# Kernel tuning notes

Hardware: AMD Instinct MI355X
Metric: run time of the kernel (lower is better)

## Reference

```python
import jax, jax.numpy as jnp
import numpy as np

N, E = 50000, 800000
D_IN, D_E = 256, 64
H1, H2 = 128, 128
N_OUT = 64
LEAKY_SLOPE = 0.01  # torch.nn.LeakyReLU default
EPS = 1e-16         # PyG softmax denominator eps


def setup_inputs() -> dict:
    key = jax.random.key(0)
    ks = jax.random.split(key, 32)

    def w(k, shape, s=0.05):
        return jax.random.normal(k, shape, dtype=jnp.float32) * s

    inp = {
        "x_in": jax.random.normal(ks[0], (N, D_IN), dtype=jnp.float32),
        "edge_index": jax.random.randint(ks[1], (2, E), 0, N),
        "edge_atts": jax.random.normal(ks[2], (E, D_E), dtype=jnp.float32),
        # TransformerConv layer 1 (in=D_IN, out=H1, heads=1, beta=True, edge_dim=D_E)
        "Wq1": w(ks[3], (H1, D_IN)), "bq1": jnp.zeros((H1,), jnp.float32),
        "Wk1": w(ks[4], (H1, D_IN)), "bk1": jnp.zeros((H1,), jnp.float32),
        "Wv1": w(ks[5], (H1, D_IN)), "bv1": jnp.zeros((H1,), jnp.float32),
        "We1": w(ks[6], (H1, D_E)),                     # lin_edge (bias=False)
        "Wskip1": w(ks[7], (H1, D_IN)), "bskip1": jnp.zeros((H1,), jnp.float32),
        "Wbeta1": w(ks[8], (1, 3 * H1)),                # lin_beta (bias=False)
        # TransformerConv layer 2 (in=H1, out=H2)
        "Wq2": w(ks[9], (H2, H1)), "bq2": jnp.zeros((H2,), jnp.float32),
        "Wk2": w(ks[10], (H2, H1)), "bk2": jnp.zeros((H2,), jnp.float32),
        "Wv2": w(ks[11], (H2, H1)), "bv2": jnp.zeros((H2,), jnp.float32),
        "We2": w(ks[12], (H2, D_E)),
        "Wskip2": w(ks[13], (H2, H1)), "bskip2": jnp.zeros((H2,), jnp.float32),
        "Wbeta2": w(ks[14], (1, 3 * H2)),
        # output MLP: Linear(H1 + H2 -> N_OUT)
        "Wm": w(ks[15], (N_OUT, H1 + H2)), "bm": jnp.zeros((N_OUT,), jnp.float32),
    }
    return inp


def _transformer_conv(x, src, dst, edge_attr,
                      Wq, bq, Wk, bk, Wv, bv, We, Wskip, bskip, Wbeta, n_nodes):
    """PyG TransformerConv: heads=1, concat=True, beta=True, root_weight=True,
    dropout inactive (eval mode)."""
    d = Wq.shape[0]
    q = x @ Wq.T + bq                      # [N, d]
    k = x @ Wk.T + bk                      # [N, d]
    v = x @ Wv.T + bv                      # [N, d]
    e = edge_attr @ We.T                   # [E, d]
    k_e = k[src] + e                       # gather source keys + edge embedding
    v_e = v[src] + e                       # gather source values + edge embedding
    # attention score per edge
    score = jnp.einsum('ed,ed->e', q[dst], k_e) / jnp.sqrt(jnp.asarray(d, jnp.float32))
    # segment softmax over incoming edges of each destination node
    m = jax.ops.segment_max(score, dst, num_segments=n_nodes)
    m = jnp.where(jnp.isfinite(m), m, 0.0)
    ex = jnp.exp(score - m[dst])
    denom = jax.ops.segment_sum(ex, dst, num_segments=n_nodes) + EPS
    alpha = ex / denom[dst]                # [E]
    # scatter-add weighted messages
    out = jax.ops.segment_sum(alpha[:, None] * v_e, dst, num_segments=n_nodes)  # [N, d]
    # beta-gated skip connection
    x_r = x @ Wskip.T + bskip
    beta = jax.nn.sigmoid(jnp.concatenate([out, x_r, out - x_r], axis=1) @ Wbeta.T)  # [N, 1]
    return beta * x_r + (1.0 - beta) * out


def _leaky_relu(x):
    return jnp.where(x >= 0, x, LEAKY_SLOPE * x)


def reference(x_in, edge_index, edge_atts,
              Wq1, bq1, Wk1, bk1, Wv1, bv1, We1, Wskip1, bskip1, Wbeta1,
              Wq2, bq2, Wk2, bk2, Wv2, bv2, We2, Wskip2, bskip2, Wbeta2,
              Wm, bm):
    src, dst = edge_index[0], edge_index[1]
    n = x_in.shape[0]
    x1 = _leaky_relu(_transformer_conv(x_in, src, dst, edge_atts,
                                       Wq1, bq1, Wk1, bk1, Wv1, bv1, We1,
                                       Wskip1, bskip1, Wbeta1, n))
    x2 = _leaky_relu(_transformer_conv(x1, src, dst, edge_atts,
                                       Wq2, bq2, Wk2, bk2, Wv2, bv2, We2,
                                       Wskip2, bskip2, Wbeta2, n))
    out = jnp.concatenate([x1, x2], axis=1) @ Wm.T + bm   # [N, N_OUT]
    return out
```

## Files before the change

kernel.cpp:

```cpp
#include <hip/hip_runtime.h>
#include <hip/hip_bf16.h>
#include <math.h>

typedef unsigned short u16;
typedef unsigned int u32;
typedef __attribute__((ext_vector_type(8))) short bf16x8;
typedef __attribute__((ext_vector_type(4))) float f32x4;

__device__ inline u16 f2bf(float x) {
    unsigned u = __float_as_uint(x);
    unsigned r = u + 0x7fff + ((u >> 16) & 1);
    return (u16)(r >> 16);
}
__device__ inline float bf2f(u16 h) { return __uint_as_float(((unsigned)h) << 16); }
__device__ inline void bsplit(float x, u16& h, u16& l) {
    h = f2bf(x);
    float r = x - bf2f(h);
    l = f2bf(r);
}

__global__ void count_deg(const int* __restrict__ dst, int* __restrict__ cnt, int E) {
    int e = blockIdx.x * blockDim.x + threadIdx.x;
    if (e < E) atomicAdd(&cnt[dst[e]], 1);
}

__global__ __launch_bounds__(1024) void scan_a(const int* __restrict__ cnt,
                                               int* __restrict__ out,
                                               int* __restrict__ partials, int N) {
    __shared__ int sh[1024];
    int tid = threadIdx.x;
    int gid = blockIdx.x * 1024 + tid;
    int v = (gid < N) ? cnt[gid] : 0;
    sh[tid] = v;
    for (int off = 1; off < 1024; off <<= 1) {
        __syncthreads();
        int add = (tid >= off) ? sh[tid - off] : 0;
        __syncthreads();
        sh[tid] += add;
    }
    __syncthreads();
    if (gid <= N) out[gid] = sh[tid] - v;
    if (tid == 1023) partials[blockIdx.x] = sh[1023];
}

__global__ void scan_b(int* __restrict__ partials, int nb) {
    if (threadIdx.x == 0 && blockIdx.x == 0) {
        int run = 0;
        for (int i = 0; i < nb; ++i) { int t = partials[i]; partials[i] = run; run += t; }
    }
}

__global__ __launch_bounds__(1024) void scan_c(int* __restrict__ out,
                                               const int* __restrict__ partials,
                                               int* __restrict__ fillb, int N) {
    int gid = blockIdx.x * 1024 + threadIdx.x;
    if (gid <= N) {
        int v = out[gid] + partials[blockIdx.x];
        out[gid] = v;
        fillb[gid] = v;
    }
}

__global__ void fill_edges(const int* __restrict__ src, const int* __restrict__ dst,
                           int* __restrict__ fillb, int2* __restrict__ esi, int E) {
    int e = blockIdx.x * blockDim.x + threadIdx.x;
    if (e < E) {
        int d = dst[e];
        int slot = atomicAdd(&fillb[d], 1);
        esi[slot] = make_int2(src[e], e);
    }
}

__global__ __launch_bounds__(256) void prep_weights(
    const float* __restrict__ Wq1, const float* __restrict__ Wk1,
    const float* __restrict__ Wv1, const float* __restrict__ Ws1,
    const float* __restrict__ We1,
    const float* __restrict__ bq1, const float* __restrict__ bk1,
    const float* __restrict__ bv1, const float* __restrict__ bs1,
    const float* __restrict__ Wq2, const float* __restrict__ Wk2,
    const float* __restrict__ Wv2, const float* __restrict__ Ws2,
    const float* __restrict__ We2,
    const float* __restrict__ bq2, const float* __restrict__ bk2,
    const float* __restrict__ bv2, const float* __restrict__ bs2,
    const float* __restrict__ Wm,
    u16* __restrict__ Wc1H, u16* __restrict__ Wc1L,
    u16* __restrict__ Wc2H, u16* __restrict__ Wc2L,
    float* __restrict__ bcat1, float* __restrict__ bcat2,
    float* __restrict__ WeT1, float* __restrict__ WeT2,
    u16* __restrict__ WmH, u16* __restrict__ WmL) {
    int b = blockIdx.x;
    int t = threadIdx.x;
    if (b < 1152) {
        int L = b / 576;
        int r = b - L * 576;
        int K = L ? 128 : 256;
        const float* Wq = L ? Wq2 : Wq1;
        const float* We = L ? We2 : We1;
        u16* WH = L ? Wc2H : Wc1H;
        u16* WL = L ? Wc2L : Wc1L;
        float* bcat = L ? bcat2 : bcat1;
        float val = 0.f;
        bool have = t < K;
        if (r < 512) {
            int sub = r >> 7, rr = r & 127;
            const float* Wsrc = L ? (sub == 0 ? Wq2 : sub == 1 ? Wk2 : sub == 2 ? Wv2 : Ws2)
                                  : (sub == 0 ? Wq1 : sub == 1 ? Wk1 : sub == 2 ? Wv1 : Ws1);
            if (have) val = Wsrc[(size_t)rr * K + t];
            if (t == 0) {
                const float* bsrc = L ? (sub == 0 ? bq2 : sub == 1 ? bk2 : sub == 2 ? bv2 : bs2)
                                      : (sub == 0 ? bq1 : sub == 1 ? bk1 : sub == 2 ? bv1 : bs1);
                bcat[r] = bsrc[rr];
            }
        } else {
            int o = r - 512;
            if (have) {
                float s = 0.f;
                for (int h = 0; h < 128; ++h)
                    s = fmaf(We[h * 64 + o], Wq[(size_t)h * K + t], s);
                val = s;
            }
            if (t == 0) {
                const float* bq = L ? bq2 : bq1;
                float sb = 0.f;
                for (int h = 0; h < 128; ++h) sb = fmaf(We[h * 64 + o], bq[h], sb);
                bcat[r] = sb;
            }
        }
        if (have) {
            u16 h, l;
            bsplit(val, h, l);
            WH[(size_t)r * K + t] = h;
            WL[(size_t)r * K + t] = l;
        }
    } else if (b == 1152 || b == 1153) {
        const float* We = (b == 1152) ? We1 : We2;
        float* WeT = (b == 1152) ? WeT1 : WeT2;
        for (int i = t; i < 128 * 64; i += 256)
            WeT[(i & 63) * 128 + (i >> 6)] = We[i];
    } else {
        for (int i = t; i < 64 * 256; i += 256) {
            u16 h, l;
            bsplit(Wm[i], h, l);
            WmH[i] = h;
            WmL[i] = l;
        }
    }
}

__global__ void split_planes(const float* __restrict__ src, u16* __restrict__ hi,
                             u16* __restrict__ lo, int n4) {
    int i = (blockIdx.x * blockDim.x + threadIdx.x) * 4;
    if (i < n4) {
        float4 v = *reinterpret_cast<const float4*>(&src[i]);
        u16 h0, h1, h2, h3, l0, l1, l2, l3;
        bsplit(v.x, h0, l0); bsplit(v.y, h1, l1);
        bsplit(v.z, h2, l2); bsplit(v.w, h3, l3);
        *reinterpret_cast<ushort4*>(&hi[i]) = make_ushort4(h0, h1, h2, h3);
        *reinterpret_cast<ushort4*>(&lo[i]) = make_ushort4(l0, l1, l2, l3);
    }
}

#define BM 128
#define BO 64
#define BKX 64
#define LSTR 72
__global__ __launch_bounds__(256) void gemm_mfma(
    const u16* __restrict__ XH, const u16* __restrict__ XL, int ldx,
    const u16* __restrict__ WH, const u16* __restrict__ WL,
    const float* __restrict__ bias, float* __restrict__ Out, int ldo,
    int Nrows, int K) {
    __shared__ __align__(16) u16 XsH[BM * LSTR];
    __shared__ __align__(16) u16 XsL[BM * LSTR];
    __shared__ __align__(16) u16 WsH[BO * LSTR];
    __shared__ __align__(16) u16 WsL[BO * LSTR];
    int n0 = blockIdx.x * BM, o0 = blockIdx.y * BO;
    int t = threadIdx.x, wid = t >> 6, lane = t & 63;
    int xr = t >> 1, xk = (t & 1) * 32;
    int wr = t >> 2, wk = (t & 3) * 16;
    bool xok = (n0 + xr) < Nrows;
    const u16* xh = XH + (size_t)(n0 + xr) * ldx + xk;
    const u16* xl = XL + (size_t)(n0 + xr) * ldx + xk;
    const u16* wh = WH + (size_t)(o0 + wr) * K + wk;
    const u16* wl = WL + (size_t)(o0 + wr) * K + wk;
    f32x4 acc[2][4] = {};
    for (int k0 = 0; k0 < K; k0 += BKX) {
#pragma unroll
        for (int j = 0; j < 4; ++j) {
            bf16x8 vh = {0, 0, 0, 0, 0, 0, 0, 0};
            bf16x8 vl = {0, 0, 0, 0, 0, 0, 0, 0};
            if (xok) {
                vh = *reinterpret_cast<const bf16x8*>(xh + k0 + 8 * j);
                vl = *reinterpret_cast<const bf16x8*>(xl + k0 + 8 * j);
            }
            *reinterpret_cast<bf16x8*>(&XsH[xr * LSTR + xk + 8 * j]) = vh;
            *reinterpret_cast<bf16x8*>(&XsL[xr * LSTR + xk + 8 * j]) = vl;
        }
#pragma unroll
        for (int j = 0; j < 2; ++j) {
            *reinterpret_cast<bf16x8*>(&WsH[wr * LSTR + wk + 8 * j]) =
                *reinterpret_cast<const bf16x8*>(wh + k0 + 8 * j);
            *reinterpret_cast<bf16x8*>(&WsL[wr * LSTR + wk + 8 * j]) =
                *reinterpret_cast<const bf16x8*>(wl + k0 + 8 * j);
        }
        __syncthreads();
#pragma unroll
        for (int kc = 0; kc < 2; ++kc) {
            int kf = kc * 32 + (lane >> 4) * 8;
            int ar = wid * 32 + (lane & 15);
            bf16x8 aH0 = *reinterpret_cast<const bf16x8*>(&XsH[ar * LSTR + kf]);
            bf16x8 aH1 = *reinterpret_cast<const bf16x8*>(&XsH[(ar + 16) * LSTR + kf]);
            bf16x8 aL0 = *reinterpret_cast<const bf16x8*>(&XsL[ar * LSTR + kf]);
            bf16x8 aL1 = *reinterpret_cast<const bf16x8*>(&XsL[(ar + 16) * LSTR + kf]);
#pragma unroll
            for (int c = 0; c < 4; ++c) {
                int br = c * 16 + (lane & 15);
                bf16x8 bH = *reinterpret_cast<const bf16x8*>(&WsH[br * LSTR + kf]);
                bf16x8 bL = *reinterpret_cast<const bf16x8*>(&WsL[br * LSTR + kf]);
                acc[0][c] = __builtin_amdgcn_mfma_f32_16x16x32_bf16(aH0, bH, acc[0][c], 0, 0, 0);
                acc[1][c] = __builtin_amdgcn_mfma_f32_16x16x32_bf16(aH1, bH, acc[1][c], 0, 0, 0);
                acc[0][c] = __builtin_amdgcn_mfma_f32_16x16x32_bf16(aH0, bL, acc[0][c], 0, 0, 0);
                acc[1][c] = __builtin_amdgcn_mfma_f32_16x16x32_bf16(aH1, bL, acc[1][c], 0, 0, 0);
                acc[0][c] = __builtin_amdgcn_mfma_f32_16x16x32_bf16(aL0, bH, acc[0][c], 0, 0, 0);
                acc[1][c] = __builtin_amdgcn_mfma_f32_16x16x32_bf16(aL1, bH, acc[1][c], 0, 0, 0);
            }
        }
        __syncthreads();
    }
#pragma unroll
    for (int c = 0; c < 4; ++c) {
        int col = o0 + c * 16 + (lane & 15);
        float bb = bias ? bias[col] : 0.f;
#pragma unroll
        for (int r = 0; r < 2; ++r) {
            int rb = n0 + wid * 32 + r * 16 + (lane >> 4) * 4;
#pragma unroll
            for (int q = 0; q < 4; ++q) {
                int row = rb + q;
                if (row < Nrows) Out[(size_t)row * ldo + col] = acc[r][c][q] + bb;
            }
        }
    }
}

__global__ __launch_bounds__(256) void pack_attn(float* __restrict__ QKVS, int Nn) {
    int gwid = (blockIdx.x * blockDim.x + threadIdx.x) >> 6;
    int lane = threadIdx.x & 63;
    int nw = (gridDim.x * blockDim.x) >> 6;
    for (int n = gwid; n < Nn; n += nw) {
        float* row = QKVS + (size_t)n * 576;
        float k0 = row[128 + lane], k1 = row[192 + lane];
        float v0 = row[256 + lane], v1 = row[320 + lane];
        u32 vp = ((u32)f2bf(v1) << 16) | (u32)f2bf(v0);
        *reinterpret_cast<float2*>(&row[128 + 2 * lane]) = make_float2(k0, k1);
        reinterpret_cast<u32*>(row)[256 + lane] = vp;
    }
}

#define AB5 8
__global__ __launch_bounds__(256) void attn5(
    const int* __restrict__ row_ptr, const int2* __restrict__ esi,
    const float* __restrict__ QKVS, const float* __restrict__ Ae,
    float* __restrict__ Acc, int Nn) {
    int t = threadIdx.x;
    int wid = t >> 6, lane = t & 63;
    const float RS2 = 0.088388347648318447f * 1.4426950408889634f;
    for (int n = blockIdx.x * 4 + wid; n < Nn; n += gridDim.x * 4) {
        int r0 = row_ptr[n], r1 = row_ptr[n + 1];
        const float* qrow = QKVS + (size_t)n * 576;
        float q0  = qrow[lane];
        float q1  = qrow[64 + lane];
        float qe0 = qrow[512 + lane];
        float m = -1e30f, l = 0.f, av0 = 0.f, av1 = 0.f, aa = 0.f;
        for (int p = r0; p < r1; p += AB5) {
            int2 se[AB5];
#pragma unroll
            for (int i = 0; i < AB5; ++i) {
                int pp = (p + i < r1) ? p + i : r1 - 1;
                se[i] = esi[pp];
            }
            float2 kp[AB5];
            u32 vu[AB5];
            float af[AB5];
#pragma unroll
            for (int i = 0; i < AB5; ++i)
                kp[i] = *reinterpret_cast<const float2*>(
                    &QKVS[(size_t)se[i].x * 576 + 128 + 2 * lane]);
#pragma unroll
            for (int i = 0; i < AB5; ++i)
                vu[i] = reinterpret_cast<const u32*>(
                    QKVS + (size_t)se[i].x * 576)[256 + lane];
#pragma unroll
            for (int i = 0; i < AB5; ++i) af[i] = Ae[(size_t)se[i].y * 64 + lane];
            float d[AB5];
#pragma unroll
            for (int i = 0; i < AB5; ++i)
                d[i] = fmaf(q0, kp[i].x, fmaf(q1, kp[i].y, qe0 * af[i]));
#pragma unroll
            for (int off = 32; off; off >>= 1) {
#pragma unroll
                for (int i = 0; i < AB5; ++i) d[i] += __shfl_xor(d[i], off, 64);
            }
            float sc[AB5];
#pragma unroll
            for (int i = 0; i < AB5; ++i) sc[i] = (p + i < r1) ? d[i] * RS2 : -1e30f;
            float bm = sc[0];
#pragma unroll
            for (int i = 1; i < AB5; ++i) bm = fmaxf(bm, sc[i]);
            float mn = fmaxf(m, bm);
            float scale = exp2f(m - mn);
            float w[AB5];
#pragma unroll
            for (int i = 0; i < AB5; ++i) w[i] = exp2f(sc[i] - mn);
            float ws = ((w[0] + w[1]) + (w[2] + w[3])) + ((w[4] + w[5]) + (w[6] + w[7]));
            l = fmaf(l, scale, ws);
            float s_aa = 0.f, s0 = 0.f, s1 = 0.f;
#pragma unroll
            for (int i = 0; i < AB5; ++i) {
                float v0 = __uint_as_float(vu[i] << 16);
                float v1 = __uint_as_float(vu[i] & 0xffff0000u);
                s_aa = fmaf(w[i], af[i], s_aa);
                s0   = fmaf(w[i], v0, s0);
                s1   = fmaf(w[i], v1, s1);
            }
            aa  = fmaf(aa,  scale, s_aa);
            av0 = fmaf(av0, scale, s0);
            av1 = fmaf(av1, scale, s1);
            m = mn;
        }
        float inv = 1.0f / (l + 1e-16f);
        float* arow = Acc + (size_t)n * 192;
        arow[lane]       = av0 * inv;
        arow[64 + lane]  = av1 * inv;
        arow[128 + lane] = aa * inv;
    }
}

__global__ __launch_bounds__(256) void epilogue_k(
    const float* __restrict__ Acc, const float* __restrict__ QKVS,
    const float* __restrict__ WeT, const float* __restrict__ Wbeta,
    u16* __restrict__ XoH, u16* __restrict__ XoL, int coff, int Nn) {
    __shared__ float WeS[64 * 128];
    __shared__ float wbA[128], wbB[128];
    int t = threadIdx.x;
    for (int i = t; i < 64 * 128; i += 256) WeS[i] = WeT[i];
    if (t < 128) {
        float w3 = Wbeta[256 + t];
        wbA[t] = Wbeta[t] + w3;
        wbB[t] = Wbeta[128 + t] - w3;
    }
    __syncthreads();
    int wid = t >> 6, lane = t & 63;
    for (int n = blockIdx.x * 4 + wid; n < Nn; n += gridDim.x * 4) {
        const float* ar = Acc + (size_t)n * 192;
        float out0 = ar[lane], out1 = ar[64 + lane], aa = ar[128 + lane];
#pragma unroll
        for (int j = 0; j < 64; ++j) {
            float aj = __shfl(aa, j, 64);
            out0 = fmaf(aj, WeS[j * 128 + lane], out0);
            out1 = fmaf(aj, WeS[j * 128 + 64 + lane], out1);
        }
        const float* qrow = QKVS + (size_t)n * 576;
        float xr0 = qrow[384 + lane], xr1 = qrow[448 + lane];
        float bp = wbA[lane] * out0 + wbA[64 + lane] * out1 +
                   wbB[lane] * xr0  + wbB[64 + lane] * xr1;
#pragma unroll
        for (int off = 32; off; off >>= 1) bp += __shfl_xor(bp, off, 64);
        float beta = 1.0f / (1.0f + __expf(-bp));
        float x0 = beta * xr0 + (1.0f - beta) * out0;
        float x1 = beta * xr1 + (1.0f - beta) * out1;
        x0 = (x0 >= 0.f) ? x0 : 0.01f * x0;
        x1 = (x1 >= 0.f) ? x1 : 0.01f * x1;
        u16 h, l16;
        size_t base = (size_t)n * 256 + coff;
        bsplit(x0, h, l16); XoH[base + lane] = h;      XoL[base + lane] = l16;
        bsplit(x1, h, l16); XoH[base + 64 + lane] = h; XoL[base + 64 + lane] = l16;
    }
}

extern "C" void kernel_launch(void* const* d_in, const int* in_sizes, int n_in,
                              void* d_out, int out_size, void* d_ws, size_t ws_size,
                              hipStream_t stream) {
    const float* x_in  = (const float*)d_in[0];
    const int*   eidx  = (const int*)d_in[1];
    const float* eatt  = (const float*)d_in[2];
    const float* Wq1 = (const float*)d_in[3];  const float* bq1 = (const float*)d_in[4];
    const float* Wk1 = (const float*)d_in[5];  const float* bk1 = (const float*)d_in[6];
    const float* Wv1 = (const float*)d_in[7];  const float* bv1 = (const float*)d_in[8];
    const float* We1 = (const float*)d_in[9];
    const float* Wskip1 = (const float*)d_in[10]; const float* bskip1 = (const float*)d_in[11];
    const float* Wbeta1 = (const float*)d_in[12];
    const float* Wq2 = (const float*)d_in[13]; const float* bq2 = (const float*)d_in[14];
    const float* Wk2 = (const float*)d_in[15]; const float* bk2 = (const float*)d_in[16];
    const float* Wv2 = (const float*)d_in[17]; const float* bv2 = (const float*)d_in[18];
    const float* We2 = (const float*)d_in[19];
    const float* Wskip2 = (const float*)d_in[20]; const float* bskip2 = (const float*)d_in[21];
    const float* Wbeta2 = (const float*)d_in[22];
    const float* Wm  = (const float*)d_in[23]; const float* bm  = (const float*)d_in[24];

    const int N = in_sizes[0] / 256;
    const int E = in_sizes[1] / 2;
    const int* srcp = eidx;
    const int* dstp = eidx + E;

    char* p = (char*)d_ws;
    auto alloc = [&](size_t bytes) -> void* {
        void* r = (void*)p;
        p += (bytes + 255) & ~(size_t)255;
        return r;
    };
    int*   row_ptr  = (int*)alloc((size_t)(N + 1) * 4);
    int*   fillb    = (int*)alloc((size_t)(N + 1) * 4);
    int*   partials = (int*)alloc(256 * 4);
    int2*  esi      = (int2*)alloc((size_t)E * 8);
    float* QKVS = (float*)alloc((size_t)N * 576 * 4);
    float* Accb = (float*)alloc((size_t)N * 192 * 4);
    u16*   XpH  = (u16*)alloc((size_t)N * 256 * 2);
    u16*   XpL  = (u16*)alloc((size_t)N * 256 * 2);
    float* WeT1 = (float*)alloc((size_t)64 * 128 * 4);
    float* WeT2 = (float*)alloc((size_t)64 * 128 * 4);
    u16*   Wc1H = (u16*)alloc((size_t)576 * 256 * 2);
    u16*   Wc1L = (u16*)alloc((size_t)576 * 256 * 2);
    u16*   Wc2H = (u16*)alloc((size_t)576 * 128 * 2);
    u16*   Wc2L = (u16*)alloc((size_t)576 * 128 * 2);
    float* bcat1 = (float*)alloc(576 * 4);
    float* bcat2 = (float*)alloc(576 * 4);
    u16*   WmH  = (u16*)alloc((size_t)64 * 256 * 2);
    u16*   WmL  = (u16*)alloc((size_t)64 * 256 * 2);

    hipMemsetAsync(fillb, 0, (size_t)(N + 1) * 4, stream);
    count_deg<<<(E + 255) / 256, 256, 0, stream>>>(dstp, fillb, E);
    int nScanBlocks = (N + 1 + 1023) / 1024;
    scan_a<<<nScanBlocks, 1024, 0, stream>>>(fillb, row_ptr, partials, N);
    scan_b<<<1, 1, 0, stream>>>(partials, nScanBlocks);
    scan_c<<<nScanBlocks, 1024, 0, stream>>>(row_ptr, partials, fillb, N);
    fill_edges<<<(E + 255) / 256, 256, 0, stream>>>(srcp, dstp, fillb, esi, E);

    prep_weights<<<1155, 256, 0, stream>>>(
        Wq1, Wk1, Wv1, Wskip1, We1, bq1, bk1, bv1, bskip1,
        Wq2, Wk2, Wv2, Wskip2, We2, bq2, bk2, bv2, bskip2, Wm,
        Wc1H, Wc1L, Wc2H, Wc2L, bcat1, bcat2, WeT1, WeT2, WmH, WmL);

    split_planes<<<(N * 256 / 4 + 255) / 256, 256, 0, stream>>>(x_in, XpH, XpL, N * 256);

    dim3 blk(256);
    int gmx = (N + BM - 1) / BM;

    gemm_mfma<<<dim3(gmx, 9), blk, 0, stream>>>(XpH, XpL, 256, Wc1H, Wc1L, bcat1,
                                                QKVS, 576, N, 256);
    pack_attn<<<2048, blk, 0, stream>>>(QKVS, N);
    attn5<<<2048, blk, 0, stream>>>(row_ptr, esi, QKVS, eatt, Accb, N);
    epilogue_k<<<1024, blk, 0, stream>>>(Accb, QKVS, WeT1, Wbeta1, XpH, XpL, 0, N);

    gemm_mfma<<<dim3(gmx, 9), blk, 0, stream>>>(XpH, XpL, 256, Wc2H, Wc2L, bcat2,
                                                QKVS, 576, N, 128);
    pack_attn<<<2048, blk, 0, stream>>>(QKVS, N);
    attn5<<<2048, blk, 0, stream>>>(row_ptr, esi, QKVS, eatt, Accb, N);
    epilogue_k<<<1024, blk, 0, stream>>>(Accb, QKVS, WeT2, Wbeta2, XpH, XpL, 128, N);

    gemm_mfma<<<dim3(gmx, 1), blk, 0, stream>>>(XpH, XpL, 256, WmH, WmL, bm,
                                                (float*)d_out, 64, N, 256);
}
```

Before: 1.057 ms.

## Fuse input split and K/V packing into GEMM, pre-permute bf16 edge attributes

The input bf16 hi/lo split now happens inside the first GEMM's tile load, so the separate split_planes pass and its planes buffer traffic go away. The K and V weight rows are interleaved so the GEMM epilogue writes keys already paired and values directly as bf16, which removes the pack_attn kernel. During CSR construction, edge attributes are permuted into destination order and stored as bf16, so the attention kernel reads them contiguously at half the bytes. The cost is a one-time scatter of the edge attributes, extra conversion work in the GEMM loader, and lower precision on the edge attributes.

```diff
diff --git a/kernel.cpp b/kernel.cpp
--- a/kernel.cpp
+++ b/kernel.cpp
@@ -61,13 +61,22 @@
     }
 }
 
-__global__ void fill_edges(const int* __restrict__ src, const int* __restrict__ dst,
-                           int* __restrict__ fillb, int2* __restrict__ esi, int E) {
-    int e = blockIdx.x * blockDim.x + threadIdx.x;
-    if (e < E) {
-        int d = dst[e];
-        int slot = atomicAdd(&fillb[d], 1);
-        esi[slot] = make_int2(src[e], e);
+__global__ __launch_bounds__(256) void fill_edges_perm(
+    const int* __restrict__ src, const int* __restrict__ dst,
+    int* __restrict__ fillb, int* __restrict__ esrc,
+    const float* __restrict__ Ae, u16* __restrict__ Aep, int E) {
+    int gwid = (blockIdx.x * blockDim.x + threadIdx.x) >> 6;
+    int lane = threadIdx.x & 63;
+    int nw = (gridDim.x * blockDim.x) >> 6;
+    for (int e = gwid; e < E; e += nw) {
+        int slot = 0;
+        if (lane == 0) {
+            int d = dst[e];
+            slot = atomicAdd(&fillb[d], 1);
+            esrc[slot] = src[e];
+        }
+        slot = __shfl(slot, 0, 64);
+        Aep[(size_t)slot * 64 + lane] = f2bf(Ae[(size_t)e * 64 + lane]);
     }
 }
 
@@ -102,14 +111,18 @@
         float val = 0.f;
         bool have = t < K;
         if (r < 512) {
-            int sub = r >> 7, rr = r & 127;
-            const float* Wsrc = L ? (sub == 0 ? Wq2 : sub == 1 ? Wk2 : sub == 2 ? Wv2 : Ws2)
-                                  : (sub == 0 ? Wq1 : sub == 1 ? Wk1 : sub == 2 ? Wv1 : Ws1);
-            if (have) val = Wsrc[(size_t)rr * K + t];
+            int srow, which;
+            if (r < 128)      { which = 0; srow = r; }
+            else if (r < 256) { which = 1; int j = r - 128; srow = (j >> 1) + (j & 1) * 64; }
+            else if (r < 384) { which = 2; int j = r - 256; srow = (j >> 1) + (j & 1) * 64; }
+            else              { which = 3; srow = r - 384; }
+            const float* Wsrc = L ? (which == 0 ? Wq2 : which == 1 ? Wk2 : which == 2 ? Wv2 : Ws2)
+                                  : (which == 0 ? Wq1 : which == 1 ? Wk1 : which == 2 ? Wv1 : Ws1);
+            if (have) val = Wsrc[(size_t)srow * K + t];
             if (t == 0) {
-                const float* bsrc = L ? (sub == 0 ? bq2 : sub == 1 ? bk2 : sub == 2 ? bv2 : bs2)
-                                      : (sub == 0 ? bq1 : sub == 1 ? bk1 : sub == 2 ? bv1 : bs1);
-                bcat[r] = bsrc[rr];
+                const float* bsrc = L ? (which == 0 ? bq2 : which == 1 ? bk2 : which == 2 ? bv2 : bs2)
+                                      : (which == 0 ? bq1 : which == 1 ? bk1 : which == 2 ? bv1 : bs1);
+                bcat[r] = bsrc[srow];
             }
         } else {
             int o = r - 512;
@@ -147,19 +160,6 @@
     }
 }
 
-__global__ void split_planes(const float* __restrict__ src, u16* __restrict__ hi,
-                             u16* __restrict__ lo, int n4) {
-    int i = (blockIdx.x * blockDim.x + threadIdx.x) * 4;
-    if (i < n4) {
-        float4 v = *reinterpret_cast<const float4*>(&src[i]);
-        u16 h0, h1, h2, h3, l0, l1, l2, l3;
-        bsplit(v.x, h0, l0); bsplit(v.y, h1, l1);
-        bsplit(v.z, h2, l2); bsplit(v.w, h3, l3);
-        *reinterpret_cast<ushort4*>(&hi[i]) = make_ushort4(h0, h1, h2, h3);
-        *reinterpret_cast<ushort4*>(&lo[i]) = make_ushort4(l0, l1, l2, l3);
-    }
-}
-
 #define BM 128
 #define BO 64
 #define BKX 64
@@ -168,7 +168,7 @@
     const u16* __restrict__ XH, const u16* __restrict__ XL, int ldx,
     const u16* __restrict__ WH, const u16* __restrict__ WL,
     const float* __restrict__ bias, float* __restrict__ Out, int ldo,
-    int Nrows, int K) {
+    u16* __restrict__ Vb, int Nrows, int K) {
     __shared__ __align__(16) u16 XsH[BM * LSTR];
     __shared__ __align__(16) u16 XsL[BM * LSTR];
     __shared__ __align__(16) u16 WsH[BO * LSTR];
@@ -178,8 +178,10 @@
     int xr = t >> 1, xk = (t & 1) * 32;
     int wr = t >> 2, wk = (t & 3) * 16;
     bool xok = (n0 + xr) < Nrows;
+    const bool xf32 = (XL == nullptr);
     const u16* xh = XH + (size_t)(n0 + xr) * ldx + xk;
-    const u16* xl = XL + (size_t)(n0 + xr) * ldx + xk;
+    const u16* xl = xf32 ? nullptr : XL + (size_t)(n0 + xr) * ldx + xk;
+    const float* x32 = reinterpret_cast<const float*>(XH) + (size_t)(n0 + xr) * ldx + xk;
     const u16* wh = WH + (size_t)(o0 + wr) * K + wk;
     const u16* wl = WL + (size_t)(o0 + wr) * K + wk;
     f32x4 acc[2][4] = {};
@@ -189,8 +191,19 @@
             bf16x8 vh = {0, 0, 0, 0, 0, 0, 0, 0};
             bf16x8 vl = {0, 0, 0, 0, 0, 0, 0, 0};
             if (xok) {
-                vh = *reinterpret_cast<const bf16x8*>(xh + k0 + 8 * j);
-                vl = *reinterpret_cast<const bf16x8*>(xl + k0 + 8 * j);
+                if (xf32) {
+                    float4 p0 = *reinterpret_cast<const float4*>(x32 + k0 + 8 * j);
+                    float4 p1 = *reinterpret_cast<const float4*>(x32 + k0 + 8 * j + 4);
+                    float xf[8] = {p0.x, p0.y, p0.z, p0.w, p1.x, p1.y, p1.z, p1.w};
+                    u16 hh[8], ll[8];
+#pragma unroll
+                    for (int q = 0; q < 8; ++q) bsplit(xf[q], hh[q], ll[q]);
+                    vh = *reinterpret_cast<bf16x8*>(hh);
+                    vl = *reinterpret_cast<bf16x8*>(ll);
+                } else {
+                    vh = *reinterpret_cast<const bf16x8*>(xh + k0 + 8 * j);
+                    vl = *reinterpret_cast<const bf16x8*>(xl + k0 + 8 * j);
+                }
             }
             *reinterpret_cast<bf16x8*>(&XsH[xr * LSTR + xk + 8 * j]) = vh;
             *reinterpret_cast<bf16x8*>(&XsL[xr * LSTR + xk + 8 * j]) = vl;
@@ -236,47 +249,45 @@
 #pragma unroll
             for (int q = 0; q < 4; ++q) {
                 int row = rb + q;
-                if (row < Nrows) Out[(size_t)row * ldo + col] = acc[r][c][q] + bb;
-            }
-        }
-    }
-}
-
-__global__ __launch_bounds__(256) void pack_attn(float* __restrict__ QKVS, int Nn) {
-    int gwid = (blockIdx.x * blockDim.x + threadIdx.x) >> 6;
-    int lane = threadIdx.x & 63;
-    int nw = (gridDim.x * blockDim.x) >> 6;
-    for (int n = gwid; n < Nn; n += nw) {
-        float* row = QKVS + (size_t)n * 576;
-        float k0 = row[128 + lane], k1 = row[192 + lane];
-        float v0 = row[256 + lane], v1 = row[320 + lane];
-        u32 vp = ((u32)f2bf(v1) << 16) | (u32)f2bf(v0);
-        *reinterpret_cast<float2*>(&row[128 + 2 * lane]) = make_float2(k0, k1);
-        reinterpret_cast<u32*>(row)[256 + lane] = vp;
+                if (row < Nrows) {
+                    float val = acc[r][c][q] + bb;
+                    if (Vb == nullptr) {
+                        Out[(size_t)row * ldo + col] = val;
+                    } else if (col < 256) {
+                        Out[(size_t)row * 448 + col] = val;
+                    } else if (col < 384) {
+                        Vb[(size_t)row * 128 + (col - 256)] = f2bf(val);
+                    } else {
+                        Out[(size_t)row * 448 + col - 128] = val;
+                    }
+                }
+            }
+        }
     }
 }
 
 #define AB5 8
-__global__ __launch_bounds__(256) void attn5(
-    const int* __restrict__ row_ptr, const int2* __restrict__ esi,
-    const float* __restrict__ QKVS, const float* __restrict__ Ae,
-    float* __restrict__ Acc, int Nn) {
+__global__ __launch_bounds__(256) void attn6(
+    const int* __restrict__ row_ptr, const int* __restrict__ esrc,
+    const float* __restrict__ A1, const u16* __restrict__ Vb,
+    const u16* __restrict__ Aep, float* __restrict__ Acc, int Nn) {
     int t = threadIdx.x;
     int wid = t >> 6, lane = t & 63;
+    const u32* Vb32 = reinterpret_cast<const u32*>(Vb);
     const float RS2 = 0.088388347648318447f * 1.4426950408889634f;
     for (int n = blockIdx.x * 4 + wid; n < Nn; n += gridDim.x * 4) {
         int r0 = row_ptr[n], r1 = row_ptr[n + 1];
-        const float* qrow = QKVS + (size_t)n * 576;
+        const float* qrow = A1 + (size_t)n * 448;
         float q0  = qrow[lane];
         float q1  = qrow[64 + lane];
-        float qe0 = qrow[512 + lane];
+        float qe0 = qrow[384 + lane];
         float m = -1e30f, l = 0.f, av0 = 0.f, av1 = 0.f, aa = 0.f;
         for (int p = r0; p < r1; p += AB5) {
-            int2 se[AB5];
+            int se[AB5];
 #pragma unroll
             for (int i = 0; i < AB5; ++i) {
                 int pp = (p + i < r1) ? p + i : r1 - 1;
-                se[i] = esi[pp];
+                se[i] = esrc[pp];
             }
             float2 kp[AB5];
             u32 vu[AB5];
@@ -284,13 +295,15 @@
 #pragma unroll
             for (int i = 0; i < AB5; ++i)
                 kp[i] = *reinterpret_cast<const float2*>(
-                    &QKVS[(size_t)se[i].x * 576 + 128 + 2 * lane]);
+                    &A1[(size_t)se[i] * 448 + 128 + 2 * lane]);
 #pragma unroll
             for (int i = 0; i < AB5; ++i)
-                vu[i] = reinterpret_cast<const u32*>(
-                    QKVS + (size_t)se[i].x * 576)[256 + lane];
-#pragma unroll
-            for (int i = 0; i < AB5; ++i) af[i] = Ae[(size_t)se[i].y * 64 + lane];
+                vu[i] = Vb32[(size_t)se[i] * 64 + lane];
+#pragma unroll
+            for (int i = 0; i < AB5; ++i) {
+                int pp = (p + i < r1) ? p + i : r1 - 1;
+                af[i] = bf2f(Aep[(size_t)pp * 64 + lane]);
+            }
             float d[AB5];
 #pragma unroll
             for (int i = 0; i < AB5; ++i)
@@ -336,7 +349,7 @@
 }
 
 __global__ __launch_bounds__(256) void epilogue_k(
-    const float* __restrict__ Acc, const float* __restrict__ QKVS,
+    const float* __restrict__ Acc, const float* __restrict__ A1,
     const float* __restrict__ WeT, const float* __restrict__ Wbeta,
     u16* __restrict__ XoH, u16* __restrict__ XoL, int coff, int Nn) {
     __shared__ float WeS[64 * 128];
@@ -359,8 +372,8 @@
             out0 = fmaf(aj, WeS[j * 128 + lane], out0);
             out1 = fmaf(aj, WeS[j * 128 + 64 + lane], out1);
         }
-        const float* qrow = QKVS + (size_t)n * 576;
-        float xr0 = qrow[384 + lane], xr1 = qrow[448 + lane];
+        const float* qrow = A1 + (size_t)n * 448;
+        float xr0 = qrow[256 + lane], xr1 = qrow[320 + lane];
         float bp = wbA[lane] * out0 + wbA[64 + lane] * out1 +
                    wbB[lane] * xr0  + wbB[64 + lane] * xr1;
 #pragma unroll
@@ -411,8 +424,10 @@
     int*   row_ptr  = (int*)alloc((size_t)(N + 1) * 4);
     int*   fillb    = (int*)alloc((size_t)(N + 1) * 4);
     int*   partials = (int*)alloc(256 * 4);
-    int2*  esi      = (int2*)alloc((size_t)E * 8);
-    float* QKVS = (float*)alloc((size_t)N * 576 * 4);
+    int*   esrc     = (int*)alloc((size_t)E * 4);
+    u16*   Aep      = (u16*)alloc((size_t)E * 64 * 2);
+    float* A1   = (float*)alloc((size_t)N * 448 * 4);
+    u16*   Vb   = (u16*)alloc((size_t)N * 128 * 2);
     float* Accb = (float*)alloc((size_t)N * 192 * 4);
     u16*   XpH  = (u16*)alloc((size_t)N * 256 * 2);
     u16*   XpL  = (u16*)alloc((size_t)N * 256 * 2);
@@ -433,30 +448,26 @@
     scan_a<<<nScanBlocks, 1024, 0, stream>>>(fillb, row_ptr, partials, N);
     scan_b<<<1, 1, 0, stream>>>(partials, nScanBlocks);
     scan_c<<<nScanBlocks, 1024, 0, stream>>>(row_ptr, partials, fillb, N);
-    fill_edges<<<(E + 255) / 256, 256, 0, stream>>>(srcp, dstp, fillb, esi, E);
+    fill_edges_perm<<<4096, 256, 0, stream>>>(srcp, dstp, fillb, esrc, eatt, Aep, E);
 
     prep_weights<<<1155, 256, 0, stream>>>(
         Wq1, Wk1, Wv1, Wskip1, We1, bq1, bk1, bv1, bskip1,
         Wq2, Wk2, Wv2, Wskip2, We2, bq2, bk2, bv2, bskip2, Wm,
         Wc1H, Wc1L, Wc2H, Wc2L, bcat1, bcat2, WeT1, WeT2, WmH, WmL);
 
-    split_planes<<<(N * 256 / 4 + 255) / 256, 256, 0, stream>>>(x_in, XpH, XpL, N * 256);
-
     dim3 blk(256);
     int gmx = (N + BM - 1) / BM;
 
-    gemm_mfma<<<dim3(gmx, 9), blk, 0, stream>>>(XpH, XpL, 256, Wc1H, Wc1L, bcat1,
-                                                QKVS, 576, N, 256);
-    pack_attn<<<2048, blk, 0, stream>>>(QKVS, N);
-    attn5<<<2048, blk, 0, stream>>>(row_ptr, esi, QKVS, eatt, Accb, N);
-    epilogue_k<<<1024, blk, 0, stream>>>(Accb, QKVS, WeT1, Wbeta1, XpH, XpL, 0, N);
-
-    gemm_mfma<<<dim3(gmx, 9), blk, 0, stream>>>(XpH, XpL, 256, Wc2H, Wc2L, bcat2,
-                                                QKVS, 576, N, 128);
-    pack_attn<<<2048, blk, 0, stream>>>(QKVS, N);
-    attn5<<<2048, blk, 0, stream>>>(row_ptr, esi, QKVS, eatt, Accb, N);
-    epilogue_k<<<1024, blk, 0, stream>>>(Accb, QKVS, WeT2, Wbeta2, XpH, XpL, 128, N);
+    gemm_mfma<<<dim3(gmx, 9), blk, 0, stream>>>((const u16*)x_in, nullptr, 256,
+                                                Wc1H, Wc1L, bcat1, A1, 0, Vb, N, 256);
+    attn6<<<2048, blk, 0, stream>>>(row_ptr, esrc, A1, Vb, Aep, Accb, N);
+    epilogue_k<<<1024, blk, 0, stream>>>(Accb, A1, WeT1, Wbeta1, XpH, XpL, 0, N);
+
+    gemm_mfma<<<dim3(gmx, 9), blk, 0, stream>>>(XpH, XpL, 256,
+                                                Wc2H, Wc2L, bcat2, A1, 0, Vb, N, 128);
+    attn6<<<2048, blk, 0, stream>>>(row_ptr, esrc, A1, Vb, Aep, Accb, N);
+    epilogue_k<<<1024, blk, 0, stream>>>(Accb, A1, WeT2, Wbeta2, XpH, XpL, 128, N);
 
     gemm_mfma<<<dim3(gmx, 1), blk, 0, stream>>>(XpH, XpL, 256, WmH, WmL, bm,
-                                                (float*)d_out, 64, N, 256);
-}
+                                                (float*)d_out, 64, nullptr, N, 256);
+}
```

Result: slower. 1.191 ms (+12.7%).
